# Kernel tuning notes

Hardware: AMD Instinct MI355X
Metric: run time of the kernel (lower is better)

## Reference

```python
import jax, jax.numpy as jnp
import numpy as np

B, S, DV = 64, 200, 128
NC2, ND = 4096, 10000


def setup_inputs() -> dict:
    key = jax.random.key(0)
    ks = jax.random.split(key, 24)
    n = lambda k, shp: jax.random.normal(k, shp, dtype=jnp.float32) * 0.05
    return dict(
        c1_seq=jax.random.randint(ks[0], (B, S), 0, 1000),
        c2_seq=jax.random.randint(ks[1], (B, S), 0, NC2),
        c4_seq=jax.random.randint(ks[2], (B, S), 0, 1000),
        d_seq=jax.random.randint(ks[3], (B, S), 0, ND),
        r_seq=jax.random.randint(ks[4], (B, S), 0, 2),
        D_emb=n(ks[5], (ND, 1)),
        v_d=n(ks[6], (DV,)),
        v_c2=n(ks[7], (DV,)),
        R_emb=n(ks[8], (2, DV)),
        W_ih=n(ks[9], (3 * DV, 2 * DV)),
        W_hh=n(ks[10], (3 * DV, DV)),
        b_ih=n(ks[11], (3 * DV,)),
        b_hh=n(ks[12], (3 * DV,)),
        W1=n(ks[13], (DV, DV)), b1=n(ks[14], (DV,)),
        W2=n(ks[15], (1, DV)), b2=n(ks[16], (1,)),
        W3=n(ks[17], (DV, 3 * DV)), b3=n(ks[18], (DV,)),
        W4=n(ks[19], (1, DV)), b4=n(ks[20], (1,)),
    )


def reference(c1_seq, c2_seq, c4_seq, d_seq, r_seq, D_emb, v_d, v_c2, R_emb,
              W_ih, W_hh, b_ih, b_hh, W1, b1, W2, b2, W3, b3, W4, b4):
    # Dropout layers are identity in eval mode.
    gamma = D_emb[d_seq]                      # [B,S,1]
    v_d_seq = gamma * v_d                     # [B,S,DV]
    v_r_seq = R_emb[r_seq]                    # [B,S,DV]
    x = jnp.concatenate([v_d_seq, v_r_seq], axis=-1)  # [B,S,2DV]

    # torch-style GRU over time (batch_first). Precompute input projections.
    xW = jnp.einsum('bsi,gi->bsg', x, W_ih) + b_ih    # [B,S,3DV]

    def gru_step(h, xw_t):
        hW = h @ W_hh.T + b_hh
        xr, xz, xn = jnp.split(xw_t, 3, axis=-1)
        hr, hz, hn = jnp.split(hW, 3, axis=-1)
        r = jax.nn.sigmoid(xr + hr)
        z = jax.nn.sigmoid(xz + hz)
        n = jnp.tanh(xn + r * hn)
        h_new = (1.0 - z) * n + z * h
        return h_new, h_new

    h0 = jnp.zeros((B, DV), x.dtype)
    _, h_seq = jax.lax.scan(gru_step, h0, jnp.swapaxes(xW, 0, 1))
    h_seq = jnp.swapaxes(h_seq, 0, 1)         # [B,S,DV]

    alpha_seq = (jax.nn.relu(h_seq @ W1.T + b1) @ W2.T + b2)[..., 0]  # [B,S]

    rows = jnp.arange(B)

    def c2_step(C2, ts):
        c2_t, vd_t, vr_t = ts
        beta = jnp.take_along_axis(C2, c2_t[:, None], axis=-1)   # [B,1] gather
        v_c2_t = beta * v_c2                                     # [B,DV]
        feat = jnp.concatenate([v_c2_t, vd_t, vr_t], axis=-1)    # [B,3DV]
        new_c2 = (jax.nn.relu(feat @ W3.T + b3) @ W4.T + b4)[:, 0]
        # one-hot masked update == per-row scatter set
        C2 = C2.at[rows, c2_t].set(new_c2)
        return C2, C2

    C2_0 = jnp.zeros((B, NC2), x.dtype)
    _, C2_seq = jax.lax.scan(
        c2_step, C2_0,
        (jnp.swapaxes(c2_seq, 0, 1), jnp.swapaxes(v_d_seq, 0, 1), jnp.swapaxes(v_r_seq, 0, 1)))
    C2_seq = jnp.swapaxes(C2_seq, 0, 1)       # [B,S,NC2]

    return alpha_seq, h_seq, C2_seq
```

## Files before the change

### kernel.cpp

```cpp
#include <hip/hip_runtime.h>

namespace {
constexpr int B_ = 64, S_ = 200, DV_ = 128, NC2_ = 4096;
}

typedef float f4v __attribute__((ext_vector_type(4)));
typedef float f32x4 __attribute__((ext_vector_type(4)));
typedef _Float16 half8 __attribute__((ext_vector_type(8)));

__device__ __forceinline__ void lds_sync() {
  asm volatile("s_waitcnt lgkmcnt(0)\n\ts_barrier" ::: "memory");
}

__global__ __launch_bounds__(512, 1) void k1_main(
    const int* __restrict__ c2_seq, const int* __restrict__ d_seq,
    const int* __restrict__ r_seq, const float* __restrict__ D_emb,
    const float* __restrict__ v_d, const float* __restrict__ v_c2,
    const float* __restrict__ R_emb,
    const float* __restrict__ W_ih, const float* __restrict__ W_hh,
    const float* __restrict__ b_ih, const float* __restrict__ b_hh,
    const float* __restrict__ W1, const float* __restrict__ b1,
    const float* __restrict__ W2, const float* __restrict__ b2,
    const float* __restrict__ W3, const float* __restrict__ b3,
    const float* __restrict__ W4, const float* __restrict__ b4,
    float* __restrict__ out_alpha, float* __restrict__ out_h,
    float* __restrict__ out_c2)
{
  __shared__ __align__(16) char smem[18944 + 208 * DV_ * 2];
  const int tid = threadIdx.x;

  if (blockIdx.x < B_) {
    const int b = blockIdx.x;
    _Float16* hist = reinterpret_cast<_Float16*>(smem);
    float* gl = reinterpret_cast<float*>(smem + 512);
    int* rl = reinterpret_cast<int*>(smem + 1312);
    float* u_l = reinterpret_cast<float*>(smem + 2112);
    float* p0_l = u_l + 384;
    float* p1_l = p0_l + 384;
    float* bh_l = p1_l + 384;
    _Float16* fullh = reinterpret_cast<_Float16*>(smem + 18944);

    for (int i = tid; i < S_; i += 512) {
      gl[i] = D_emb[d_seq[b * S_ + i]];
      rl[i] = r_seq[b * S_ + i];
    }
    if (tid < 256) reinterpret_cast<_Float16*>(hist)[tid] = (_Float16)0.f;
    {
      uint* fz = reinterpret_cast<uint*>(fullh + 200 * DV_);
      for (int i = tid; i < 8 * DV_ / 2; i += 512) fz[i] = 0u;
    }

    if (tid < 384) {
      const int row = tid;
      const float4* wi =
          reinterpret_cast<const float4*>(W_ih + (size_t)row * 2 * DV_);
      const float4* vd4 = reinterpret_cast<const float4*>(v_d);
      const float4* re4 = reinterpret_cast<const float4*>(R_emb);
      float uu = 0.f, pp0 = 0.f, pp1 = 0.f;
#pragma unroll 8
      for (int k = 0; k < DV_ / 4; ++k) {
        float4 a = wi[k], vv = vd4[k];
        uu += a.x * vv.x + a.y * vv.y + a.z * vv.z + a.w * vv.w;
        float4 c = wi[DV_ / 4 + k];
        float4 r0 = re4[k], r1 = re4[DV_ / 4 + k];
        pp0 += c.x * r0.x + c.y * r0.y + c.z * r0.z + c.w * r0.w;
        pp1 += c.x * r1.x + c.y * r1.y + c.z * r1.z + c.w * r1.w;
      }
      const float bi = b_ih[row];
      u_l[row] = uu; p0_l[row] = pp0 + bi; p1_l[row] = pp1 + bi;
      bh_l[row] = b_hh[row];
    }

    const int w = tid >> 6, l = tid & 63;
    const int col = l & 15, kg = l >> 4;
    const int d = 16 * w + col;
    half8 bf[3][4];
#pragma unroll
    for (int g = 0; g < 3; ++g) {
      const float* wr = W_hh + (size_t)(g * DV_ + d) * DV_;
#pragma unroll
      for (int kt = 0; kt < 4; ++kt) {
        const int k0 = kt * 32 + kg * 8;
        const float4 lo = *reinterpret_cast<const float4*>(wr + k0);
        const float4 hi = *reinterpret_cast<const float4*>(wr + k0 + 4);
        half8 hb;
        hb[0] = (_Float16)lo.x; hb[1] = (_Float16)lo.y;
        hb[2] = (_Float16)lo.z; hb[3] = (_Float16)lo.w;
        hb[4] = (_Float16)hi.x; hb[5] = (_Float16)hi.y;
        hb[6] = (_Float16)hi.z; hb[7] = (_Float16)hi.w;
        bf[g][kt] = hb;
      }
    }
    __syncthreads();

    float u3[3], p03[3], p13[3], bh3[3];
#pragma unroll
    for (int g = 0; g < 3; ++g) {
      u3[g] = u_l[g * DV_ + d];
      p03[g] = p0_l[g * DV_ + d];
      p13[g] = p1_l[g * DV_ + d];
      bh3[g] = bh_l[g * DV_ + d];
    }
    float hprev = 0.f;
    float gv = gl[0];
    int rv = rl[0];

    float* outp = out_h + (size_t)b * S_ * DV_ + d;
    for (int t = 0; t < S_; ++t) {
      const int cur = t & 1;
      half8 af[4];
#pragma unroll
      for (int kt = 0; kt < 4; ++kt)
        af[kt] = *reinterpret_cast<const half8*>(&hist[cur * DV_ + kt * 32 + kg * 8]);
      f32x4 a0 = {0.f, 0.f, 0.f, 0.f}, a1 = a0, a2 = a0;
#pragma unroll
      for (int kt = 0; kt < 4; ++kt) {
        a0 = __builtin_amdgcn_mfma_f32_16x16x32_f16(af[kt], bf[0][kt], a0, 0, 0, 0);
        a1 = __builtin_amdgcn_mfma_f32_16x16x32_f16(af[kt], bf[1][kt], a1, 0, 0, 0);
        a2 = __builtin_amdgcn_mfma_f32_16x16x32_f16(af[kt], bf[2][kt], a2, 0, 0, 0);
      }
      const float xr = gv * u3[0] + (rv ? p13[0] : p03[0]);
      const float xz = gv * u3[1] + (rv ? p13[1] : p03[1]);
      const float xn = gv * u3[2] + (rv ? p13[2] : p03[2]);
      const float r = 1.f / (1.f + __expf(-(xr + a0[0] + bh3[0])));
      const float z = 1.f / (1.f + __expf(-(xz + a1[0] + bh3[1])));
      const float nx = xn + r * (a2[0] + bh3[2]);
      const float e2 = __expf(2.f * nx);
      const float n = (e2 - 1.f) / (e2 + 1.f);
      const float hnew = (1.f - z) * n + z * hprev;
      hprev = hnew;
      if (kg == 0) {
        outp[(size_t)t * DV_] = hnew;
        const _Float16 hf = (_Float16)hnew;
        hist[(cur ^ 1) * DV_ + d] = hf;
        fullh[t * DV_ + (d ^ ((t & 7) << 3))] = hf;
      }
      if (t + 1 < S_) { gv = gl[t + 1]; rv = rl[t + 1]; }
      lds_sync();
    }

    half8 bf1[4];
    {
      const float* wr1 = W1 + (size_t)d * DV_;
#pragma unroll
      for (int kt = 0; kt < 4; ++kt) {
        const int k0 = kt * 32 + kg * 8;
        const float4 lo = *reinterpret_cast<const float4*>(wr1 + k0);
        const float4 hi = *reinterpret_cast<const float4*>(wr1 + k0 + 4);
        half8 hb;
        hb[0] = (_Float16)lo.x; hb[1] = (_Float16)lo.y;
        hb[2] = (_Float16)lo.z; hb[3] = (_Float16)lo.w;
        hb[4] = (_Float16)hi.x; hb[5] = (_Float16)hi.y;
        hb[6] = (_Float16)hi.z; hb[7] = (_Float16)hi.w;
        bf1[kt] = hb;
      }
    }
    const float b1v = b1[d], w2v = W2[d], b2v = b2[0];
    float* alphaAcc = u_l;
    if (tid < 208) alphaAcc[tid] = b2v;
    lds_sync();
    for (int st = 0; st < 13; ++st) {
      const int row = 16 * st + col;
      half8 af2[4];
#pragma unroll
      for (int kt = 0; kt < 4; ++kt) {
        const int c0 = (kt * 32 + kg * 8) ^ ((row & 7) << 3);
        af2[kt] = *reinterpret_cast<const half8*>(&fullh[row * DV_ + c0]);
      }
      f32x4 y = {0.f, 0.f, 0.f, 0.f};
#pragma unroll
      for (int kt = 0; kt < 4; ++kt)
        y = __builtin_amdgcn_mfma_f32_16x16x32_f16(af2[kt], bf1[kt], y, 0, 0, 0);
#pragma unroll
      for (int j = 0; j < 4; ++j) {
        float part = w2v * fmaxf(y[j] + b1v, 0.f);
        part += __shfl_xor(part, 1);
        part += __shfl_xor(part, 2);
        part += __shfl_xor(part, 4);
        part += __shfl_xor(part, 8);
        if (col == 0) atomicAdd(&alphaAcc[16 * st + 4 * kg + j], part);
      }
    }
    lds_sync();
    if (tid < S_) out_alpha[b * S_ + tid] = alphaAcc[tid];
  } else {
    const int b = blockIdx.x - B_;
    float* a3s = reinterpret_cast<float*>(smem);
    float* u3s = a3s + DV_;
    float* q0s = u3s + DV_;
    float* q1s = q0s + DV_;
    float* w4s = q1s + DV_;
    float* vals = w4s + DV_;
    float* gl = vals + S_;
    int* rl = reinterpret_cast<int*>(gl + S_);
    int* jl = rl + S_;
    int* prevs = jl + S_;
    int* done = prevs + S_;
    int* nresp = done + S_;

    if (tid == 0) *nresp = 0;
    for (int i = tid; i < S_; i += 512) {
      gl[i] = D_emb[d_seq[b * S_ + i]];
      rl[i] = r_seq[b * S_ + i];
      jl[i] = c2_seq[b * S_ + i];
      done[i] = 0;
    }
    if (tid < DV_) {
      const int d = tid;
      const float4* w3r = reinterpret_cast<const float4*>(W3 + (size_t)d * 3 * DV_);
      const float4* vc4 = reinterpret_cast<const float4*>(v_c2);
      const float4* vd4 = reinterpret_cast<const float4*>(v_d);
      const float4* re4 = reinterpret_cast<const float4*>(R_emb);
      float a3 = 0, u3 = 0, q0 = 0, q1 = 0;
#pragma unroll 8
      for (int k = 0; k < DV_ / 4; ++k) {
        float4 a = w3r[k], cc = vc4[k];
        a3 += a.x * cc.x + a.y * cc.y + a.z * cc.z + a.w * cc.w;
        float4 u = w3r[DV_ / 4 + k], dd = vd4[k];
        u3 += u.x * dd.x + u.y * dd.y + u.z * dd.z + u.w * dd.w;
        float4 cq = w3r[2 * (DV_ / 4) + k];
        float4 r0 = re4[k], r1 = re4[DV_ / 4 + k];
        q0 += cq.x * r0.x + cq.y * r0.y + cq.z * r0.z + cq.w * r0.w;
        q1 += cq.x * r1.x + cq.y * r1.y + cq.z * r1.z + cq.w * r1.w;
      }
      const float bb = b3[d];
      a3s[d] = a3; u3s[d] = u3; q0s[d] = q0 + bb; q1s[d] = q1 + bb;
      w4s[d] = W4[d];
    }
    __syncthreads();
    if (tid < S_) {
      const int jj = jl[tid];
      int p = -1;
      for (int q = tid - 1; q >= 0; --q)
        if (jl[q] == jj) { p = q; break; }
      prevs[tid] = p;
    }
    const float b4v = b4[0];
    __syncthreads();

    const int t = tid;
    const float gv = (t < S_) ? gl[t] : 0.f;
    const int rv = (t < S_) ? rl[t] : 0;
    const int p = (t < S_) ? prevs[t] : -1;
    bool mine_done = (t >= S_);

    for (int round = 0; round < S_; ++round) {
      float myval = 0.f;
      bool computed = false;
      if (!mine_done && (p < 0 || done[p])) {
        const float beta = (p < 0) ? 0.f : vals[p];
        const float4* a34 = reinterpret_cast<const float4*>(a3s);
        const float4* u34 = reinterpret_cast<const float4*>(u3s);
        const float4* q04 = reinterpret_cast<const float4*>(q0s);
        const float4* q14 = reinterpret_cast<const float4*>(q1s);
        const float4* w44 = reinterpret_cast<const float4*>(w4s);
        float acc = 0.f;
#pragma unroll 8
        for (int k = 0; k < DV_ / 4; ++k) {
          float4 a = a34[k], u = u34[k];
          float4 q = rv ? q14[k] : q04[k];
          float4 ww = w44[k];
          float h0 = beta * a.x + gv * u.x + q.x;
          float h1 = beta * a.y + gv * u.y + q.y;
          float h2 = beta * a.z + gv * u.z + q.z;
          float h3 = beta * a.w + gv * u.w + q.w;
          acc += ww.x * fmaxf(h0, 0.f) + ww.y * fmaxf(h1, 0.f) +
                 ww.z * fmaxf(h2, 0.f) + ww.w * fmaxf(h3, 0.f);
        }
        myval = acc + b4v;
        computed = true;
      }
      __syncthreads();
      if (computed) {
        vals[t] = myval;
        done[t] = 1;
        mine_done = true;
        atomicAdd(nresp, 1);
      }
      __syncthreads();
      if (*nresp >= S_) break;
    }
    __syncthreads();

    f4v v0 = {0.f, 0.f, 0.f, 0.f}, v1 = v0;
    f4v* dst4 = reinterpret_cast<f4v*>(out_c2 + (size_t)b * S_ * NC2_);
    for (int s = 0; s < S_; ++s) {
      const int j_ = jl[s];
      const int f_ = j_ >> 2;
      if ((f_ & 511) == tid) {
        const float vv_ = vals[s];
        const int rr_ = f_ >> 9, q_ = j_ & 3;
        if (rr_ == 0) {
          if (q_ == 0) v0.x = vv_; else if (q_ == 1) v0.y = vv_;
          else if (q_ == 2) v0.z = vv_; else v0.w = vv_;
        } else {
          if (q_ == 0) v1.x = vv_; else if (q_ == 1) v1.y = vv_;
          else if (q_ == 2) v1.z = vv_; else v1.w = vv_;
        }
      }
      f4v* drow = dst4 + (size_t)s * (NC2_ / 4);
      __builtin_nontemporal_store(v0, drow + tid);
      __builtin_nontemporal_store(v1, drow + tid + 512);
    }
  }
}

extern "C" void kernel_launch(void* const* d_in, const int* in_sizes, int n_in,
                              void* d_out, int out_size, void* d_ws, size_t ws_size,
                              hipStream_t stream) {
  const int* c2_seq = (const int*)d_in[1];
  const int* d_seq = (const int*)d_in[3];
  const int* r_seq = (const int*)d_in[4];
  const float* D_emb = (const float*)d_in[5];
  const float* v_d = (const float*)d_in[6];
  const float* v_c2 = (const float*)d_in[7];
  const float* R_emb = (const float*)d_in[8];
  const float* W_ih = (const float*)d_in[9];
  const float* W_hh = (const float*)d_in[10];
  const float* b_ih = (const float*)d_in[11];
  const float* b_hh = (const float*)d_in[12];
  const float* W1 = (const float*)d_in[13];
  const float* b1 = (const float*)d_in[14];
  const float* W2 = (const float*)d_in[15];
  const float* b2 = (const float*)d_in[16];
  const float* W3 = (const float*)d_in[17];
  const float* b3 = (const float*)d_in[18];
  const float* W4 = (const float*)d_in[19];
  const float* b4 = (const float*)d_in[20];

  float* out = (float*)d_out;
  float* out_alpha = out;
  float* out_h = out + B_ * S_;
  float* out_c2 = out + B_ * S_ + (size_t)B_ * S_ * DV_;

  k1_main<<<dim3(2 * B_), dim3(512), 0, stream>>>(
      c2_seq, d_seq, r_seq, D_emb, v_d, v_c2, R_emb, W_ih, W_hh, b_ih, b_hh,
      W1, b1, W2, b2, W3, b3, W4, b4, out_alpha, out_h, out_c2);
}
```

Baseline: 134.3 us.

## Interleave alpha MLP into GRU loop and split C2 writeout across two blocks

```diff
diff --git a/kernel.cpp b/kernel.cpp
--- a/kernel.cpp
+++ b/kernel.cpp
@@ -26,7 +26,7 @@
     float* __restrict__ out_alpha, float* __restrict__ out_h,
     float* __restrict__ out_c2)
 {
-  __shared__ __align__(16) char smem[18944 + 208 * DV_ * 2];
+  __shared__ __align__(16) char smem[18944 + 208 * DV_ * 2 + 8 * 208 * 4];
   const int tid = threadIdx.x;
 
   if (blockIdx.x < B_) {
@@ -39,6 +39,7 @@
     float* p1_l = p0_l + 384;
     float* bh_l = p1_l + 384;
     _Float16* fullh = reinterpret_cast<_Float16*>(smem + 18944);
+    float* strips = reinterpret_cast<float*>(smem + 18944 + 208 * DV_ * 2);
 
     for (int i = tid; i < S_; i += 512) {
       gl[i] = D_emb[d_seq[b * S_ + i]];
@@ -91,6 +92,23 @@
         bf[g][kt] = hb;
       }
     }
+    half8 bf1[4];
+    {
+      const float* wr1 = W1 + (size_t)d * DV_;
+#pragma unroll
+      for (int kt = 0; kt < 4; ++kt) {
+        const int k0 = kt * 32 + kg * 8;
+        const float4 lo = *reinterpret_cast<const float4*>(wr1 + k0);
+        const float4 hi = *reinterpret_cast<const float4*>(wr1 + k0 + 4);
+        half8 hb;
+        hb[0] = (_Float16)lo.x; hb[1] = (_Float16)lo.y;
+        hb[2] = (_Float16)lo.z; hb[3] = (_Float16)lo.w;
+        hb[4] = (_Float16)hi.x; hb[5] = (_Float16)hi.y;
+        hb[6] = (_Float16)hi.z; hb[7] = (_Float16)hi.w;
+        bf1[kt] = hb;
+      }
+    }
+    const float b1v = b1[d], w2v = W2[d];
     __syncthreads();
 
     float u3[3], p03[3], p13[3], bh3[3];
@@ -107,6 +125,29 @@
 
     float* outp = out_h + (size_t)b * S_ * DV_ + d;
     for (int t = 0; t < S_; ++t) {
+      if ((t & 15) == 0 && t >= 16) {
+        const int st = (t >> 4) - 1;
+        const int row = 16 * st + col;
+        half8 af2[4];
+#pragma unroll
+        for (int kt = 0; kt < 4; ++kt) {
+          const int c0 = (kt * 32 + kg * 8) ^ ((row & 7) << 3);
+          af2[kt] = *reinterpret_cast<const half8*>(&fullh[row * DV_ + c0]);
+        }
+        f32x4 y = {0.f, 0.f, 0.f, 0.f};
+#pragma unroll
+        for (int kt = 0; kt < 4; ++kt)
+          y = __builtin_amdgcn_mfma_f32_16x16x32_f16(af2[kt], bf1[kt], y, 0, 0, 0);
+#pragma unroll
+        for (int j = 0; j < 4; ++j) {
+          float part = w2v * fmaxf(y[j] + b1v, 0.f);
+          part += __shfl_xor(part, 1);
+          part += __shfl_xor(part, 2);
+          part += __shfl_xor(part, 4);
+          part += __shfl_xor(part, 8);
+          if (col == 0) strips[w * 208 + 16 * st + 4 * kg + j] = part;
+        }
+      }
       const int cur = t & 1;
       half8 af[4];
 #pragma unroll
@@ -139,27 +180,8 @@
       lds_sync();
     }
 
-    half8 bf1[4];
     {
-      const float* wr1 = W1 + (size_t)d * DV_;
-#pragma unroll
-      for (int kt = 0; kt < 4; ++kt) {
-        const int k0 = kt * 32 + kg * 8;
-        const float4 lo = *reinterpret_cast<const float4*>(wr1 + k0);
-        const float4 hi = *reinterpret_cast<const float4*>(wr1 + k0 + 4);
-        half8 hb;
-        hb[0] = (_Float16)lo.x; hb[1] = (_Float16)lo.y;
-        hb[2] = (_Float16)lo.z; hb[3] = (_Float16)lo.w;
-        hb[4] = (_Float16)hi.x; hb[5] = (_Float16)hi.y;
-        hb[6] = (_Float16)hi.z; hb[7] = (_Float16)hi.w;
-        bf1[kt] = hb;
-      }
-    }
-    const float b1v = b1[d], w2v = W2[d], b2v = b2[0];
-    float* alphaAcc = u_l;
-    if (tid < 208) alphaAcc[tid] = b2v;
-    lds_sync();
-    for (int st = 0; st < 13; ++st) {
+      const int st = 12;
       const int row = 16 * st + col;
       half8 af2[4];
 #pragma unroll
@@ -178,13 +200,21 @@
         part += __shfl_xor(part, 2);
         part += __shfl_xor(part, 4);
         part += __shfl_xor(part, 8);
-        if (col == 0) atomicAdd(&alphaAcc[16 * st + 4 * kg + j], part);
+        if (col == 0) strips[w * 208 + 16 * st + 4 * kg + j] = part;
       }
     }
     lds_sync();
-    if (tid < S_) out_alpha[b * S_ + tid] = alphaAcc[tid];
+    const float b2v = b2[0];
+    for (int i = tid; i < S_; i += 512) {
+      float s = b2v;
+#pragma unroll
+      for (int ww = 0; ww < 8; ++ww) s += strips[ww * 208 + i];
+      out_alpha[b * S_ + i] = s;
+    }
   } else {
-    const int b = blockIdx.x - B_;
+    const int fb = blockIdx.x - B_;
+    const int b = fb >> 1, half = fb & 1;
+    const int s0 = half * 100;
     float* a3s = reinterpret_cast<float*>(smem);
     float* u3s = a3s + DV_;
     float* q0s = u3s + DV_;
@@ -283,25 +313,34 @@
     __syncthreads();
 
     f4v v0 = {0.f, 0.f, 0.f, 0.f}, v1 = v0;
+
+#define APPLY_EVT(T)                                                          \
+    {                                                                         \
+      const int j_ = jl[(T)];                                                 \
+      const int f_ = j_ >> 2;                                                 \
+      if ((f_ & 511) == tid) {                                                \
+        const float vv_ = vals[(T)];                                          \
+        const int rr_ = f_ >> 9, q_ = j_ & 3;                                 \
+        if (rr_ == 0) {                                                       \
+          if (q_ == 0) v0.x = vv_; else if (q_ == 1) v0.y = vv_;              \
+          else if (q_ == 2) v0.z = vv_; else v0.w = vv_;                      \
+        } else {                                                              \
+          if (q_ == 0) v1.x = vv_; else if (q_ == 1) v1.y = vv_;              \
+          else if (q_ == 2) v1.z = vv_; else v1.w = vv_;                      \
+        }                                                                     \
+      }                                                                       \
+    }
+
+    for (int tt = 0; tt < s0; ++tt) APPLY_EVT(tt);
+
     f4v* dst4 = reinterpret_cast<f4v*>(out_c2 + (size_t)b * S_ * NC2_);
-    for (int s = 0; s < S_; ++s) {
-      const int j_ = jl[s];
-      const int f_ = j_ >> 2;
-      if ((f_ & 511) == tid) {
-        const float vv_ = vals[s];
-        const int rr_ = f_ >> 9, q_ = j_ & 3;
-        if (rr_ == 0) {
-          if (q_ == 0) v0.x = vv_; else if (q_ == 1) v0.y = vv_;
-          else if (q_ == 2) v0.z = vv_; else v0.w = vv_;
-        } else {
-          if (q_ == 0) v1.x = vv_; else if (q_ == 1) v1.y = vv_;
-          else if (q_ == 2) v1.z = vv_; else v1.w = vv_;
-        }
-      }
+    for (int s = s0; s < s0 + 100; ++s) {
+      APPLY_EVT(s);
       f4v* drow = dst4 + (size_t)s * (NC2_ / 4);
       __builtin_nontemporal_store(v0, drow + tid);
       __builtin_nontemporal_store(v1, drow + tid + 512);
     }
+#undef APPLY_EVT
   }
 }
 
@@ -333,7 +372,7 @@
   float* out_h = out + B_ * S_;
   float* out_c2 = out + B_ * S_ + (size_t)B_ * S_ * DV_;
 
-  k1_main<<<dim3(2 * B_), dim3(512), 0, stream>>>(
+  k1_main<<<dim3(B_ + 2 * B_), dim3(512), 0, stream>>>(
       c2_seq, d_seq, r_seq, D_emb, v_d, v_c2, R_emb, W_ih, W_hh, b_ih, b_hh,
       W1, b1, W2, b2, W3, b3, W4, b4, out_alpha, out_h, out_c2);
 }
```

Result: slower. 141.8 us (+5.6%).
